# Optimization experiments

Measured on AMD Instinct MI355X. Metric: run time of the kernel, lower is better.

## Reference

```python
import jax, jax.numpy as jnp
import numpy as np

N = 100000       # num nodes
E = 1600000      # num edges (avg degree 16)
IN_DIM = 256
EMB_DIM = 128
K = 2            # nlayers: number of propagation steps


def setup_inputs() -> dict:
    key = jax.random.key(0)
    k1, k2, k3, k4, k5 = jax.random.split(key, 5)
    x = jax.random.normal(k1, (N, IN_DIM), dtype=jnp.float32)
    # glorot-initialized linear weight + zero bias
    scale = jnp.sqrt(6.0 / (IN_DIM + EMB_DIM))
    W = jax.random.uniform(k2, (IN_DIM, EMB_DIM), minval=-scale, maxval=scale, dtype=jnp.float32)
    b = jnp.zeros((EMB_DIM,), dtype=jnp.float32)
    edge_src = jax.random.randint(k3, (E,), 0, N, dtype=jnp.int32)
    edge_dst = jax.random.randint(k4, (E,), 0, N, dtype=jnp.int32)
    # normalized-adjacency-like edge weights (positive, ~1/deg scale)
    edge_w = jax.random.uniform(k5, (E,), dtype=jnp.float32) * (1.0 / 16.0)
    return {"x": x, "W": W, "b": b, "edge_src": edge_src, "edge_dst": edge_dst, "edge_w": edge_w}


def reference(x, W, b, edge_src, edge_dst, edge_w):
    # dropout is identity in eval mode; linear + relu
    h = jax.nn.relu(x @ W + b)  # [N, EMB_DIM]
    # k-step sparse propagation: h <- g @ h, g given as COO edge list
    for _ in range(K):
        msg = h[edge_src] * edge_w[:, None]                     # [E, EMB_DIM]
        h = jax.ops.segment_sum(msg, edge_dst, num_segments=N)  # [N, EMB_DIM]
    return h
```

## Files before the change

kernel.cpp:

```cpp
#include <hip/hip_runtime.h>

#define IN_DIM 256
#define EMB 128
#define BKT_SHIFT 9
#define BKT_NODES 512
#define BINE 2048
#define SCAP 12288

typedef __attribute__((ext_vector_type(8))) short short8;
typedef __attribute__((ext_vector_type(4))) float f32x4;

__device__ __forceinline__ unsigned short bf16rtne(float f) {
    unsigned int u = __float_as_uint(f);
    return (unsigned short)((u + 0x7fffu + ((u >> 16) & 1u)) >> 16);
}

__device__ __forceinline__ unsigned int packbf2(float lo, float hi) {
    return ((unsigned int)bf16rtne(hi) << 16) | (unsigned int)bf16rtne(lo);
}

__device__ __forceinline__ short8 pack8(float4 f0, float4 f1) {
    union { uint4 u; short8 s; } U;
    asm("v_cvt_pk_bf16_f32 %0, %1, %2" : "=v"(U.u.x) : "v"(f0.x), "v"(f0.y));
    asm("v_cvt_pk_bf16_f32 %0, %1, %2" : "=v"(U.u.y) : "v"(f0.z), "v"(f0.w));
    asm("v_cvt_pk_bf16_f32 %0, %1, %2" : "=v"(U.u.z) : "v"(f1.x), "v"(f1.y));
    asm("v_cvt_pk_bf16_f32 %0, %1, %2" : "=v"(U.u.w) : "v"(f1.z), "v"(f1.w));
    return U.s;
}


__global__ __launch_bounds__(256) void bin_scatter(const int* __restrict__ src,
                                                   const int* __restrict__ dst,
                                                   const float* __restrict__ w,
                                                   int* __restrict__ gcursor,
                                                   int2* __restrict__ binned, int E,
                                                   const float* __restrict__ W,
                                                   unsigned short* __restrict__ wtg) {
    __shared__ int h[256];
    __shared__ int gbase[256];
    __shared__ int lcur[256];
    int t = threadIdx.x;

    if (blockIdx.x == 0) {
        for (int i = t; i < IN_DIM * EMB; i += 256) {
            int c = i & 127;
            int k = i >> 7;
            wtg[c * 256 + k] = bf16rtne(W[(size_t)k * 128 + c]);
        }
    }

    int e0 = blockIdx.x * BINE;
    int e1 = min(E, e0 + BINE);
    int n = e1 - e0;

    int ed[8], es[8];
    float ewv[8];
    if (n == BINE) {
#pragma unroll
        for (int j = 0; j < 8; ++j) {
            int i = e0 + t + j * 256;
            ed[j] = dst[i];
            es[j] = src[i];
            ewv[j] = w[i];
        }
    } else {
#pragma unroll
        for (int j = 0; j < 8; ++j) {
            int i = e0 + t + j * 256;
            if (i < e1) {
                ed[j] = dst[i];
                es[j] = src[i];
                ewv[j] = w[i];
            } else
                ed[j] = -1;
        }
    }
    h[t] = 0;
    lcur[t] = 0;
    __syncthreads();
#pragma unroll
    for (int j = 0; j < 8; ++j)
        if (ed[j] >= 0) atomicAdd(&h[ed[j] >> BKT_SHIFT], 1);
    __syncthreads();
    int v = h[t];
    gbase[t] = v ? atomicAdd(&gcursor[t], v) : 0;
    __syncthreads();
#pragma unroll
    for (int j = 0; j < 8; ++j) {
        if (ed[j] >= 0) {
            int b = ed[j] >> BKT_SHIFT;
            int p = gbase[b] + atomicAdd(&lcur[b], 1);
            if (p < SCAP) {
                int2 r;
                r.x = es[j] | ((ed[j] & (BKT_NODES - 1)) << 17);
                r.y = __float_as_int(ewv[j]);
                binned[(size_t)b * SCAP + p] = r;
            }
        }
    }
}


__global__ __launch_bounds__(1024) void bucket_sort(const int2* __restrict__ binned,
                                                    const int* __restrict__ counts,
                                                    int2* __restrict__ sorted,
                                                    int* __restrict__ row_ptr,
                                                    int N, int E, int NB) {
    __shared__ int cnt[BKT_NODES];
    __shared__ int cur[BKT_NODES];
    __shared__ int scn[BKT_NODES];
    __shared__ int sc[256];
    __shared__ int begS, nS;
    __shared__ int2 stage[SCAP];
    int t = threadIdx.x;
    int b = blockIdx.x;
    int node0 = b << BKT_SHIFT;
    int nn = min(BKT_NODES, N - node0);

    if (t < 256) sc[t] = (t < NB) ? min(counts[t], SCAP) : 0;
    __syncthreads();
    for (int off = 1; off < 256; off <<= 1) {
        int u = 0;
        if (t < 256 && t >= off) u = sc[t - off];
        __syncthreads();
        if (t < 256) sc[t] += u;
        __syncthreads();
    }
    if (t == 0) {
        int cb = min(counts[b], SCAP);
        begS = sc[b] - cb;
        nS = cb;
        if (b == 0) row_ptr[N] = E;
    }
    __syncthreads();
    int beg = begS;
    int n = nS;

    if (t < BKT_NODES) cnt[t] = 0;
    __syncthreads();
    const int2* bsrc = binned + (size_t)b * SCAP;
    for (int i = t; i < n; i += 1024) {
        int ld = ((unsigned int)bsrc[i].x) >> 17;
        atomicAdd(&cnt[ld], 1);
    }
    __syncthreads();
    int v = 0;
    if (t < BKT_NODES) {
        v = cnt[t];
        scn[t] = v;
    }
    __syncthreads();
    for (int off = 1; off < BKT_NODES; off <<= 1) {
        int u = 0;
        if (t < BKT_NODES && t >= off) u = scn[t - off];
        __syncthreads();
        if (t < BKT_NODES) scn[t] += u;
        __syncthreads();
    }
    if (t < BKT_NODES) {
        int excl = scn[t] - v;
        cur[t] = excl;
        if (t < nn) row_ptr[node0 + t] = beg + excl;
    }
    __syncthreads();
    for (int i = t; i < n; i += 1024) {
        int2 r = bsrc[i];
        int ld = ((unsigned int)r.x) >> 17;
        int p = atomicAdd(&cur[ld], 1);
        r.x &= 0x1FFFF;
        stage[p] = r;
    }
    __syncthreads();
    for (int i = t; i < n; i += 1024) sorted[beg + i] = stage[i];
}


__global__ __launch_bounds__(256) void gemm_mfma(const float* __restrict__ x,
                                                 const unsigned short* __restrict__ wtg,
                                                 const float* __restrict__ bias,
                                                 unsigned short* __restrict__ hbf, int N) {
    __shared__ float Asf[128][64];
    __shared__ unsigned short Bs[128][64];
    int tid = threadIdx.x;
    int wv = tid >> 6;
    int lane = tid & 63;
    int lr = lane & 15;
    int lg = lane >> 4;
    int wr = wv * 32;
    int row0 = blockIdx.x * 128;

    f32x4 acc[2][8];
#pragma unroll
    for (int m = 0; m < 2; ++m)
#pragma unroll
        for (int n = 0; n < 8; ++n) acc[m][n] = (f32x4){0.f, 0.f, 0.f, 0.f};

    for (int kb = 0; kb < IN_DIM; kb += 64) {
#pragma unroll
        for (int i = 0; i < 8; ++i) {
            int p = 256 * i + wv * 64 + lane;
            int r = p >> 4;
            int c = p & 15;
            int gr = row0 + r;
            if (gr >= N) gr = N - 1;
            const float* ga = x + (size_t)gr * IN_DIM + kb + ((c ^ (r & 7)) << 2);
            __builtin_amdgcn_global_load_lds(
                (const __attribute__((address_space(1))) void*)ga,
                (__attribute__((address_space(3))) void*)((char*)&Asf[0][0] + (size_t)(256 * i + wv * 64) * 16),
                16, 0, 0);
        }
#pragma unroll
        for (int i = 0; i < 4; ++i) {
            int p = 256 * i + wv * 64 + lane;
            int r = p >> 3;
            int c = p & 7;
            const unsigned short* gb = wtg + (size_t)r * IN_DIM + kb + ((c ^ (r & 7)) * 8);
            __builtin_amdgcn_global_load_lds(
                (const __attribute__((address_space(1))) void*)gb,
                (__attribute__((address_space(3))) void*)((char*)&Bs[0][0] + (size_t)(256 * i + wv * 64) * 16),
                16, 0, 0);
        }
        __syncthreads();

        short8 a[2][2];
#pragma unroll
        for (int m = 0; m < 2; ++m)
#pragma unroll
            for (int kk = 0; kk < 2; ++kk) {
                int r = wr + m * 16 + lr;
                int s = r & 7;
                int ch0 = kk * 8 + lg * 2;
                float4 f0 = *(const float4*)&Asf[r][(ch0 ^ s) << 2];
                float4 f1 = *(const float4*)&Asf[r][((ch0 + 1) ^ s) << 2];
                a[m][kk] = pack8(f0, f1);
            }
#pragma unroll
        for (int n = 0; n < 8; ++n) {
            int cc = n * 16 + lr;
            int sw = cc & 7;
            short8 b0 = *(const short8*)&Bs[cc][(((0 * 4 + lg) ^ sw) * 8)];
            short8 b1 = *(const short8*)&Bs[cc][(((1 * 4 + lg) ^ sw) * 8)];
            acc[0][n] = __builtin_amdgcn_mfma_f32_16x16x32_bf16(a[0][0], b0, acc[0][n], 0, 0, 0);
            acc[0][n] = __builtin_amdgcn_mfma_f32_16x16x32_bf16(a[0][1], b1, acc[0][n], 0, 0, 0);
            acc[1][n] = __builtin_amdgcn_mfma_f32_16x16x32_bf16(a[1][0], b0, acc[1][n], 0, 0, 0);
            acc[1][n] = __builtin_amdgcn_mfma_f32_16x16x32_bf16(a[1][1], b1, acc[1][n], 0, 0, 0);
        }
        __syncthreads();
    }

#pragma unroll
    for (int n = 0; n < 8; ++n) {
        int c = n * 16 + lr;
        float bv = bias[c];
#pragma unroll
        for (int m = 0; m < 2; ++m) {
#pragma unroll
            for (int j = 0; j < 4; ++j) {
                int r = row0 + wr + m * 16 + lg * 4 + j;
                if (r < N) {
                    float v = fmaxf(acc[m][n][j] + bv, 0.f);
                    hbf[(size_t)r * EMB + c] = bf16rtne(v);
                }
            }
        }
    }
}


template <int OUTBF>
__global__ __launch_bounds__(256) void prop_g(const unsigned int* __restrict__ hin,
                                              void* __restrict__ hout,
                                              const int* __restrict__ rp,
                                              const int2* __restrict__ rec, int N) {
    int wvid = threadIdx.x >> 6;
    int lane = threadIdx.x & 63;
    int node = blockIdx.x * 4 + wvid;
    if (node >= N) return;
    int beg = __builtin_amdgcn_readfirstlane(rp[node]);
    int end = __builtin_amdgcn_readfirstlane(rp[node + 1]);
    float ax = 0.f, ay = 0.f;
    for (int c0 = beg; c0 < end; c0 += 64) {
        int cnt = end - c0;
        if (cnt > 64) cnt = 64;
        int li = lane < cnt ? lane : 0;
        int2 r = rec[c0 + li];
        for (int jb = 0; jb < cnt; jb += 16) {
            int ssrc[16];
            float sw[16];
#pragma unroll
            for (int k = 0; k < 16; ++k) {
                int jj = jb + k;
                int jc = jj < cnt ? jj : 0;
                ssrc[k] = __builtin_amdgcn_readlane(r.x, jc);
                float wv = __uint_as_float((unsigned int)__builtin_amdgcn_readlane(r.y, jc));
                sw[k] = (jj < cnt) ? wv : 0.f;
            }
            unsigned int g[16];
#pragma unroll
            for (int k = 0; k < 16; ++k) g[k] = hin[(size_t)ssrc[k] * 64 + lane];
#pragma unroll
            for (int k = 0; k < 16; ++k) {
                ax = fmaf(sw[k], __uint_as_float(g[k] << 16), ax);
                ay = fmaf(sw[k], __uint_as_float(g[k] & 0xffff0000u), ay);
            }
        }
    }
    if (OUTBF) {
        ((unsigned int*)hout)[(size_t)node * 64 + lane] = packbf2(ax, ay);
    } else {
        float2 o;
        o.x = ax;
        o.y = ay;
        ((float2*)hout)[(size_t)node * 64 + lane] = o;
    }
}


extern "C" void kernel_launch(void* const* d_in, const int* in_sizes, int n_in,
                              void* d_out, int out_size, void* d_ws, size_t ws_size,
                              hipStream_t stream) {
    const float* x = (const float*)d_in[0];
    const float* W = (const float*)d_in[1];
    const float* b = (const float*)d_in[2];
    const int* esrc = (const int*)d_in[3];
    const int* edst = (const int*)d_in[4];
    const float* ew = (const float*)d_in[5];
    int N = in_sizes[0] / IN_DIM;
    int E = in_sizes[3];
    int NB = (N + BKT_NODES - 1) >> BKT_SHIFT;

    char* p = (char*)d_ws;
    auto alloc = [&](size_t bytes) -> void* {
        void* r = (void*)p;
        p += (bytes + 255) & ~(size_t)255;
        return r;
    };
    unsigned short* hbf = (unsigned short*)alloc((size_t)N * EMB * 2);
    unsigned short* h1bf = (unsigned short*)alloc((size_t)N * EMB * 2);
    unsigned short* wtg = (unsigned short*)alloc((size_t)IN_DIM * EMB * 2);
    int* gcursor = (int*)alloc(256 * 4);
    int* row_ptr = (int*)alloc((size_t)(N + 1) * 4);
    int2* binned = (int2*)alloc((size_t)NB * SCAP * 8);
    int2* sorted = (int2*)alloc((size_t)E * 8);

    hipMemsetAsync(gcursor, 0, 256 * 4, stream);
    bin_scatter<<<(E + BINE - 1) / BINE, 256, 0, stream>>>(esrc, edst, ew, gcursor, binned, E, W, wtg);
    bucket_sort<<<NB, 1024, 0, stream>>>(binned, gcursor, sorted, row_ptr, N, E, NB);

    gemm_mfma<<<(N + 127) / 128, 256, 0, stream>>>(x, wtg, b, hbf, N);
    prop_g<1><<<(N + 3) / 4, 256, 0, stream>>>((const unsigned int*)hbf, h1bf, row_ptr, sorted, N);
    prop_g<0><<<(N + 3) / 4, 256, 0, stream>>>((const unsigned int*)h1bf, d_out, row_ptr, sorted, N);
}
```

Before: 233.7 us.

## Replace global atomic bucket cursors with histogram, column scan, deterministic scatter

Binning now runs as three passes: a per-block histogram of destination buckets, a per-bucket exclusive scan across blocks, and a scatter that writes at the precomputed offsets. This removes the contended global atomicAdd on the bucket cursors and the memset before it, and makes the order of binned edges deterministic. Blocks grow to 512 threads with 4096 edges each. The cost is reading the dst array twice, two extra kernel launches, and a scan that caps the number of blocks at 512.

Result: faster. 222.7 us (-4.7%).

```diff
diff --git a/kernel.cpp b/kernel.cpp
--- a/kernel.cpp
+++ b/kernel.cpp
@@ -4,7 +4,7 @@
 #define EMB 128
 #define BKT_SHIFT 9
 #define BKT_NODES 512
-#define BINE 2048
+#define BINE 4096
 #define SCAP 12288
 
 typedef __attribute__((ext_vector_type(8))) short short8;
@@ -29,36 +29,78 @@
 }
 
 
-__global__ __launch_bounds__(256) void bin_scatter(const int* __restrict__ src,
-                                                   const int* __restrict__ dst,
-                                                   const float* __restrict__ w,
-                                                   int* __restrict__ gcursor,
-                                                   int2* __restrict__ binned, int E,
-                                                   const float* __restrict__ W,
-                                                   unsigned short* __restrict__ wtg) {
+__global__ __launch_bounds__(512) void bin_hist(const int* __restrict__ dst,
+                                                int* __restrict__ hm, int E,
+                                                const float* __restrict__ W,
+                                                unsigned short* __restrict__ wtg) {
     __shared__ int h[256];
-    __shared__ int gbase[256];
-    __shared__ int lcur[256];
     int t = threadIdx.x;
-
     if (blockIdx.x == 0) {
-        for (int i = t; i < IN_DIM * EMB; i += 256) {
+        for (int i = t; i < IN_DIM * EMB; i += 512) {
             int c = i & 127;
             int k = i >> 7;
             wtg[c * 256 + k] = bf16rtne(W[(size_t)k * 128 + c]);
         }
     }
-
     int e0 = blockIdx.x * BINE;
     int e1 = min(E, e0 + BINE);
     int n = e1 - e0;
-
+    int ed[8];
+    if (n == BINE) {
+#pragma unroll
+        for (int j = 0; j < 8; ++j) ed[j] = dst[e0 + t + j * 512];
+    } else {
+#pragma unroll
+        for (int j = 0; j < 8; ++j) {
+            int i = e0 + t + j * 512;
+            ed[j] = (i < e1) ? dst[i] : -1;
+        }
+    }
+    if (t < 256) h[t] = 0;
+    __syncthreads();
+#pragma unroll
+    for (int j = 0; j < 8; ++j)
+        if (ed[j] >= 0) atomicAdd(&h[ed[j] >> BKT_SHIFT], 1);
+    __syncthreads();
+    if (t < 256) hm[blockIdx.x * 256 + t] = h[t];
+}
+
+
+__global__ __launch_bounds__(512) void col_scan(int* __restrict__ hm,
+                                                int* __restrict__ counts, int nblk) {
+    __shared__ int s[512];
+    int b = blockIdx.x;
+    int t = threadIdx.x;
+    int v = (t < nblk) ? hm[t * 256 + b] : 0;
+    s[t] = v;
+    __syncthreads();
+    for (int off = 1; off < 512; off <<= 1) {
+        int u = (t >= off) ? s[t - off] : 0;
+        __syncthreads();
+        s[t] += u;
+        __syncthreads();
+    }
+    if (t < nblk) hm[t * 256 + b] = s[t] - v;
+    if (t == 511) counts[b] = s[511];
+}
+
+
+__global__ __launch_bounds__(512) void bin_scatter(const int* __restrict__ src,
+                                                   const int* __restrict__ dst,
+                                                   const float* __restrict__ w,
+                                                   const int* __restrict__ hm,
+                                                   int2* __restrict__ binned, int E) {
+    __shared__ int lcur[256];
+    int t = threadIdx.x;
+    int e0 = blockIdx.x * BINE;
+    int e1 = min(E, e0 + BINE);
+    int n = e1 - e0;
     int ed[8], es[8];
     float ewv[8];
     if (n == BINE) {
 #pragma unroll
         for (int j = 0; j < 8; ++j) {
-            int i = e0 + t + j * 256;
+            int i = e0 + t + j * 512;
             ed[j] = dst[i];
             es[j] = src[i];
             ewv[j] = w[i];
@@ -66,7 +108,7 @@
     } else {
 #pragma unroll
         for (int j = 0; j < 8; ++j) {
-            int i = e0 + t + j * 256;
+            int i = e0 + t + j * 512;
             if (i < e1) {
                 ed[j] = dst[i];
                 es[j] = src[i];
@@ -75,21 +117,13 @@
                 ed[j] = -1;
         }
     }
-    h[t] = 0;
-    lcur[t] = 0;
-    __syncthreads();
-#pragma unroll
-    for (int j = 0; j < 8; ++j)
-        if (ed[j] >= 0) atomicAdd(&h[ed[j] >> BKT_SHIFT], 1);
-    __syncthreads();
-    int v = h[t];
-    gbase[t] = v ? atomicAdd(&gcursor[t], v) : 0;
+    if (t < 256) lcur[t] = hm[blockIdx.x * 256 + t];
     __syncthreads();
 #pragma unroll
     for (int j = 0; j < 8; ++j) {
         if (ed[j] >= 0) {
             int b = ed[j] >> BKT_SHIFT;
-            int p = gbase[b] + atomicAdd(&lcur[b], 1);
+            int p = atomicAdd(&lcur[b], 1);
             if (p < SCAP) {
                 int2 r;
                 r.x = es[j] | ((ed[j] & (BKT_NODES - 1)) << 17);
@@ -328,6 +362,7 @@
     int N = in_sizes[0] / IN_DIM;
     int E = in_sizes[3];
     int NB = (N + BKT_NODES - 1) >> BKT_SHIFT;
+    int nblk = (E + BINE - 1) / BINE;
 
     char* p = (char*)d_ws;
     auto alloc = [&](size_t bytes) -> void* {
@@ -338,14 +373,16 @@
     unsigned short* hbf = (unsigned short*)alloc((size_t)N * EMB * 2);
     unsigned short* h1bf = (unsigned short*)alloc((size_t)N * EMB * 2);
     unsigned short* wtg = (unsigned short*)alloc((size_t)IN_DIM * EMB * 2);
-    int* gcursor = (int*)alloc(256 * 4);
+    int* counts = (int*)alloc(256 * 4);
     int* row_ptr = (int*)alloc((size_t)(N + 1) * 4);
+    int* hm = (int*)alloc((size_t)nblk * 256 * 4);
     int2* binned = (int2*)alloc((size_t)NB * SCAP * 8);
     int2* sorted = (int2*)alloc((size_t)E * 8);
 
-    hipMemsetAsync(gcursor, 0, 256 * 4, stream);
-    bin_scatter<<<(E + BINE - 1) / BINE, 256, 0, stream>>>(esrc, edst, ew, gcursor, binned, E, W, wtg);
-    bucket_sort<<<NB, 1024, 0, stream>>>(binned, gcursor, sorted, row_ptr, N, E, NB);
+    bin_hist<<<nblk, 512, 0, stream>>>(edst, hm, E, W, wtg);
+    col_scan<<<256, 512, 0, stream>>>(hm, counts, nblk);
+    bin_scatter<<<nblk, 512, 0, stream>>>(esrc, edst, ew, hm, binned, E);
+    bucket_sort<<<NB, 1024, 0, stream>>>(binned, counts, sorted, row_ptr, N, E, NB);
 
     gemm_mfma<<<(N + 127) / 128, 256, 0, stream>>>(x, wtg, b, hbf, N);
     prop_g<1><<<(N + 3) / 4, 256, 0, stream>>>((const unsigned int*)hbf, h1bf, row_ptr, sorted, N);
```
